# Optimization experiments

Hardware: AMD Instinct MI355X
Metric: run time of the kernel (lower is better)

Reference implementation:

```python
import jax, jax.numpy as jnp
import numpy as np

B, S, E, NH = 2, 1024, 2048, 16
DH = E // NH
EPS = 1e-6

def setup_inputs() -> dict:
    key = jax.random.key(0)
    ks = jax.random.split(key, 6)
    q = jax.random.normal(ks[0], (B, S, E), dtype=jnp.float32)
    k = jax.random.normal(ks[1], (B, S, E), dtype=jnp.float32)
    v = jax.random.normal(ks[2], (B, S, E), dtype=jnp.float32)
    Wi = jax.random.normal(ks[3], (3 * E, NH), dtype=jnp.float32) * 0.02
    bi = jax.random.normal(ks[4], (NH,), dtype=jnp.float32) * 0.1
    Wf = jax.random.normal(ks[5], (3 * E, NH), dtype=jnp.float32) * 0.02
    bf = jnp.linspace(3.0, 6.0, NH, dtype=jnp.float32)  # bias_linspace_initializer(3,6)
    ln_scale = jnp.ones((E,), dtype=jnp.float32)
    return {"q": q, "k": k, "v": v, "Wi": Wi, "bi": bi, "Wf": Wf, "bf": bf, "ln_scale": ln_scale}

def _mlstm_forward(q, k, v, Wi, bi, Wf, bf, ln_scale):
    b, s, e = q.shape
    nh = Wi.shape[1]
    dh = e // nh
    x = jnp.concatenate([q, k, v], axis=-1)                     # (B,S,3E)
    ig = (x @ Wi + bi).transpose(0, 2, 1)[..., None]            # (B,NH,S,1)
    fg = (x @ Wf + bf).transpose(0, 2, 1)[..., None]            # (B,NH,S,1)
    split = lambda t: t.reshape(b, s, nh, dh).transpose(0, 2, 1, 3)
    qh, kh, vh = split(q), split(k), split(v)                   # (B,NH,S,DH)
    # parallel_stabilized_simple backend
    log_f = jax.nn.log_sigmoid(fg)                              # (B,NH,S,1)
    log_f_cum = jnp.concatenate(
        [jnp.zeros((b, nh, 1, 1), q.dtype), jnp.cumsum(log_f, axis=2)], axis=2
    )                                                           # (B,NH,S+1,1)
    # D[i,j] = cumsum[i] - cumsum[j] on causal part
    fg_mat = log_f_cum - jnp.transpose(log_f_cum, (0, 1, 3, 2)) # (B,NH,S+1,S+1)
    ltr = jnp.tril(jnp.ones((s, s), dtype=bool))
    log_fg = jnp.where(ltr, fg_mat[:, :, 1:, 1:], -jnp.inf)     # (B,NH,S,S)
    log_D = log_fg + jnp.transpose(ig, (0, 1, 3, 2))            # + i_j per column
    max_log_D = jnp.max(log_D, axis=-1, keepdims=True)          # (B,NH,S,1)
    D = jnp.exp(log_D - max_log_D)
    qk = jnp.einsum('bhsd,bhtd->bhst', qh, kh) / jnp.sqrt(jnp.asarray(dh, q.dtype))
    C = qk * D                                                  # (B,NH,S,S)
    normalizer = jnp.maximum(jnp.abs(C.sum(-1, keepdims=True)), jnp.exp(-max_log_D))
    Cn = C / (normalizer + EPS)
    h = jnp.einsum('bhst,bhtd->bhsd', Cn, vh)                   # (B,NH,S,DH)
    # MultiHeadLayerNorm: normalize over DH per head, scale (no bias)
    mu = h.mean(-1, keepdims=True)
    var = ((h - mu) ** 2).mean(-1, keepdims=True)
    hn = (h - mu) * jax.lax.rsqrt(var + EPS)
    hn = hn * ln_scale.reshape(1, nh, 1, dh)
    return hn.transpose(0, 2, 1, 3).reshape(b, s, e)            # (B,S,E)

def reference(q, k, v, Wi, bi, Wf, bf, ln_scale):
    return _mlstm_forward(q, k, v, Wi, bi, Wf, bf, ln_scale)
```

## Files before the change

### kernel.cpp

```cpp
#include <hip/hip_runtime.h>
#include <hip/hip_bf16.h>

#define B_   2
#define S_   1024
#define E_   2048
#define NH_  16
#define DH_  128
#define EPS_ 1e-6f

using half8   = __attribute__((ext_vector_type(8))) _Float16;
using floatx4 = __attribute__((ext_vector_type(4))) float;

__device__ __forceinline__ half8 cvt8h(const float* __restrict__ p) {
    float4 a = *(const float4*)p;
    float4 b = *(const float4*)(p + 4);
    half8 r;
    r[0] = (_Float16)a.x; r[1] = (_Float16)a.y;
    r[2] = (_Float16)a.z; r[3] = (_Float16)a.w;
    r[4] = (_Float16)b.x; r[5] = (_Float16)b.y;
    r[6] = (_Float16)b.z; r[7] = (_Float16)b.w;
    return r;
}

__global__ __launch_bounds__(256, 4) void gates_kernel(
    const float* __restrict__ q, const float* __restrict__ k,
    const float* __restrict__ v, const float* __restrict__ Wi,
    const float* __restrict__ Wf, float* __restrict__ pre_i,
    float* __restrict__ pre_f, _Float16* __restrict__ qhg,
    _Float16* __restrict__ khg, _Float16* __restrict__ vtg)
{
    __shared__ __attribute__((aligned(16))) _Float16 xs[32 * 264];
    __shared__ __attribute__((aligned(16))) _Float16 wt[32 * 264];

    const int t    = threadIdx.x;
    const int w    = t >> 6, lane = t & 63, quad = lane >> 4, l15 = lane & 15;
    const int mw   = w & 1, nw = w >> 1;
    const int m0   = blockIdx.x * 32;
    const int by   = blockIdx.y;
    const int kbase = by * 768;
    const int bblk = m0 >> 10;
    const int s0   = m0 & 1023;

    floatx4 acc = {0.f, 0.f, 0.f, 0.f};

    for (int c = 0; c < 3; ++c) {
        __syncthreads();
        const int e0   = kbase + c * 256;
        const int tsel = e0 >> 11;
        const int el0  = e0 & 2047;
        const float* xb = (tsel == 0) ? q : (tsel == 1) ? k : v;
        _Float16* fout = (tsel == 0) ? qhg : khg;
        #pragma unroll
        for (int i = 0; i < 4; ++i) {
            int g = t + i * 256;
            int row = g >> 5, grp = g & 31;
            half8 s8 = cvt8h(xb + (size_t)(m0 + row) * E_ + el0 + grp * 8);
            *(half8*)(&xs[row * 264 + grp * 8]) = s8;
            if (tsel < 2) {
                int el = el0 + grp * 8;
                int h  = el >> 7, d = el & 127;
                *(half8*)(fout + ((size_t)(bblk * NH_ + h) * S_ + s0 + row) * DH_ + d) = s8;
            }
        }
        {
            const int kk = t;
            const float* wiRow = Wi + (size_t)(e0 + kk) * NH_;
            const float* wfRow = Wf + (size_t)(e0 + kk) * NH_;
            float wif[16], wff[16];
            #pragma unroll
            for (int i4 = 0; i4 < 4; ++i4) {
                float4 a = *(const float4*)(wiRow + i4 * 4);
                wif[i4*4+0]=a.x; wif[i4*4+1]=a.y; wif[i4*4+2]=a.z; wif[i4*4+3]=a.w;
                float4 b = *(const float4*)(wfRow + i4 * 4);
                wff[i4*4+0]=b.x; wff[i4*4+1]=b.y; wff[i4*4+2]=b.z; wff[i4*4+3]=b.w;
            }
            #pragma unroll
            for (int hh = 0; hh < 16; ++hh) wt[hh * 264 + kk]        = (_Float16)wif[hh];
            #pragma unroll
            for (int hh = 0; hh < 16; ++hh) wt[(16 + hh) * 264 + kk] = (_Float16)wff[hh];
        }
        __syncthreads();
        if (tsel == 2) {
            const int col = t;
            const int el  = el0 + col;
            const int h   = el >> 7, d = el & 127;
            _Float16 tmp[32];
            #pragma unroll
            for (int r = 0; r < 32; ++r) tmp[r] = xs[r * 264 + col];
            const size_t vo = ((size_t)(bblk * NH_ + h) * DH_ + d) * S_ + s0;
            #pragma unroll
            for (int i = 0; i < 4; ++i)
                *(half8*)(vtg + vo + i * 8) = *(half8*)(&tmp[i * 8]);
        }
        #pragma unroll
        for (int ks = 0; ks < 8; ++ks) {
            half8 af = *(const half8*)(&xs[(mw * 16 + l15) * 264 + ks * 32 + quad * 8]);
            half8 bw = *(const half8*)(&wt[(nw * 16 + l15) * 264 + ks * 32 + quad * 8]);
            acc = __builtin_amdgcn_mfma_f32_16x16x32_f16(af, bw, acc, 0, 0, 0);
        }
    }
    #pragma unroll
    for (int reg = 0; reg < 4; ++reg) {
        int m   = m0 + mw * 16 + quad * 4 + reg;
        int b   = m >> 10, s = m & 1023;
        int col = nw * 16 + l15;
        float vacc = acc[reg];
        if (col < 16)
            pre_i[((size_t)(by * 32 + b * NH_ + col)) * S_ + s] = vacc;
        else
            pre_f[((size_t)(by * 32 + b * NH_ + col - 16)) * S_ + s] = vacc;
    }
}

__global__ __launch_bounds__(1024, 1) void scan_kernel(
    const float* __restrict__ pre_i, const float* __restrict__ pre_f,
    float* __restrict__ Aj, float* __restrict__ Cq,
    float* __restrict__ NFo, const float* __restrict__ bi,
    const float* __restrict__ bfb)
{
    __shared__ float wsumF[16], wmaxA[16];
    const int bh   = blockIdx.x;
    const int h    = bh & 15;
    const int t    = threadIdx.x;
    const int lane = t & 63, wv = t >> 6;

    float igv = bi[h], x = bfb[h];
    #pragma unroll
    for (int y = 0; y < 8; ++y) {
        igv += pre_i[((size_t)(y * 32 + bh)) * S_ + t];
        x   += pre_f[((size_t)(y * 32 + bh)) * S_ + t];
    }
    float lfv = (x >= 0.f) ? -log1pf(__expf(-x)) : (x - log1pf(__expf(x)));

    float sc = lfv;
    #pragma unroll
    for (int off = 1; off < 64; off <<= 1) {
        float o = __shfl_up(sc, off);
        if (lane >= off) sc += o;
    }
    if (lane == 63) wsumF[wv] = sc;
    __syncthreads();
    float Foff = 0.f;
    for (int i = 0; i < wv; ++i) Foff += wsumF[i];
    float F = Foff + sc;
    float a = igv - F;

    float ms = a;
    #pragma unroll
    for (int off = 1; off < 64; off <<= 1) {
        float o = __shfl_up(ms, off);
        if (lane >= off) ms = fmaxf(ms, o);
    }
    if (lane == 63) wmaxA[wv] = ms;
    __syncthreads();
    float Moff = -3.0e38f;
    for (int i = 0; i < wv; ++i) Moff = fmaxf(Moff, wmaxA[i]);
    float M = fmaxf(Moff, ms);

    size_t o = (size_t)bh * S_ + t;
    const float L2E = 1.4426950408889634f;
    Aj[o]  = a * L2E;
    Cq[o]  = -M * L2E - 3.5f;
    NFo[o] = expf(fminf(-(F + M), 80.f));
}

__global__ __launch_bounds__(256, 2) void attn_kernel(
    const _Float16* __restrict__ qh, const _Float16* __restrict__ kh,
    const _Float16* __restrict__ vtg, const float* __restrict__ Aj,
    const float* __restrict__ Cq, const float* __restrict__ NFi,
    const float* __restrict__ lnsc, float* __restrict__ out)
{
    __shared__ __attribute__((aligned(16))) _Float16 Ks[64 * 136];
    __shared__ __attribute__((aligned(16))) _Float16 Vt[128 * 72];
    __shared__ __attribute__((aligned(16))) _Float16 Pb[64 * 72];
    __shared__ float aj[64];
    __shared__ float lpart[2][2][32];
    __shared__ float spart[2][2][32];
    __shared__ float qpart[2][2][32];

    const int t    = threadIdx.x;
    const int w    = t >> 6, lane = t & 63, quad = lane >> 4, l15 = lane & 15;
    const int mw   = w & 1, nw = w >> 1;
    const int L    = blockIdx.x;
    int qi, bh;
    if (L < 256) { qi = L >> 5;                bh = L & 31; }
    else         { qi = 15 - ((L - 256) >> 5); bh = (L - 256) & 31; }
    const int b    = bh >> 4, h = bh & 15;
    const int q0   = qi * 64;
    const int krow = t >> 2, kd0 = (t & 3) * 32;
    const int vd   = t >> 1, vj0 = (t & 1) * 32;

    float ci_r[2][4], nfv_r[2][4];
    #pragma unroll
    for (int s = 0; s < 2; ++s)
        #pragma unroll
        for (int reg = 0; reg < 4; ++reg) {
            int rl = q0 + mw * 32 + s * 16 + quad * 4 + reg;
            ci_r[s][reg]  = Cq[(size_t)bh * S_ + rl];
            nfv_r[s][reg] = NFi[(size_t)bh * S_ + rl];
        }
    half8 aq[2][4];
    #pragma unroll
    for (int s = 0; s < 2; ++s) {
        const _Float16* qrow = qh + ((size_t)bh * S_ + q0 + mw * 32 + s * 16 + l15) * DH_;
        #pragma unroll
        for (int ks = 0; ks < 4; ++ks)
            aq[s][ks] = *(const half8*)(qrow + ks * 32 + quad * 8);
    }

    half8 kreg[4], vreg[4];
    float ajreg = 0.f;
    {
        const _Float16* kp = kh + ((size_t)bh * S_ + krow) * DH_ + kd0;
        const _Float16* vp = vtg + ((size_t)bh * DH_ + vd) * S_ + vj0;
        #pragma unroll
        for (int i = 0; i < 4; ++i) { kreg[i] = *(const half8*)(kp + i * 8);
                                      vreg[i] = *(const half8*)(vp + i * 8); }
    }
    if (t < 64) ajreg = Aj[(size_t)bh * S_ + t];

    #pragma unroll
    for (int i = 0; i < 4; ++i) {
        *(half8*)(&Ks[krow * 136 + kd0 + i * 8]) = kreg[i];
        *(half8*)(&Vt[vd * 72 + vj0 + i * 8])    = vreg[i];
    }
    if (t < 64) aj[t] = ajreg;
    __syncthreads();

    floatx4 acc_h[2][4];
    #pragma unroll
    for (int s = 0; s < 2; ++s)
        #pragma unroll
        for (int i = 0; i < 4; ++i) acc_h[s][i] = (floatx4){0.f, 0.f, 0.f, 0.f};
    float lrun[2][4] = {{0.f, 0.f, 0.f, 0.f}, {0.f, 0.f, 0.f, 0.f}};

    for (int kt = 0; kt <= qi; ++kt) {
        if (kt < qi) {
            const int j0n = (kt + 1) * 64;
            const _Float16* kp = kh + ((size_t)bh * S_ + j0n + krow) * DH_ + kd0;
            const _Float16* vp = vtg + ((size_t)bh * DH_ + vd) * S_ + j0n + vj0;
            #pragma unroll
            for (int i = 0; i < 4; ++i) { kreg[i] = *(const half8*)(kp + i * 8);
                                          vreg[i] = *(const half8*)(vp + i * 8); }
            if (t < 64) ajreg = Aj[(size_t)bh * S_ + j0n + t];
        }

        const bool diag = (kt == qi);
        floatx4 sacc[2][2];
        #pragma unroll
        for (int s = 0; s < 2; ++s)
            #pragma unroll
            for (int n = 0; n < 2; ++n) sacc[s][n] = (floatx4){0.f, 0.f, 0.f, 0.f};
        if (!(diag && mw == 0 && nw == 1)) {
            __builtin_amdgcn_s_setprio(1);
            #pragma unroll
            for (int ks = 0; ks < 4; ++ks) {
                #pragma unroll
                for (int n = 0; n < 2; ++n) {
                    half8 bk = *(const half8*)(&Ks[(nw * 32 + n * 16 + l15) * 136 + ks * 32 + quad * 8]);
                    sacc[0][n] = __builtin_amdgcn_mfma_f32_16x16x32_f16(aq[0][ks], bk, sacc[0][n], 0, 0, 0);
                    sacc[1][n] = __builtin_amdgcn_mfma_f32_16x16x32_f16(aq[1][ks], bk, sacc[1][n], 0, 0, 0);
                }
            }
            __builtin_amdgcn_s_setprio(0);
        }
        #pragma unroll
        for (int n = 0; n < 2; ++n) {
            int jl = nw * 32 + n * 16 + l15;
            float a_j = aj[jl];
            #pragma unroll
            for (int s = 0; s < 2; ++s) {
                #pragma unroll
                for (int reg = 0; reg < 4; ++reg) {
                    int rloc = mw * 32 + s * 16 + quad * 4 + reg;
                    float p = 0.f;
                    if (!diag || (jl <= rloc))
                        p = sacc[s][n][reg] * exp2f(ci_r[s][reg] + a_j);
                    lrun[s][reg] += p;
                    Pb[rloc * 72 + jl] = (_Float16)p;
                }
            }
        }
        __syncthreads();

        if (kt < qi) {
            #pragma unroll
            for (int i = 0; i < 4; ++i)
                *(half8*)(&Ks[krow * 136 + kd0 + i * 8]) = kreg[i];
            if (t < 64) aj[t] = ajreg;
        }
        __builtin_amdgcn_s_setprio(1);
        #pragma unroll
        for (int ks2 = 0; ks2 < 2; ++ks2) {
            half8 ap0 = *(const half8*)(&Pb[(mw * 32 + l15) * 72 + ks2 * 32 + quad * 8]);
            half8 ap1 = *(const half8*)(&Pb[(mw * 32 + 16 + l15) * 72 + ks2 * 32 + quad * 8]);
            #pragma unroll
            for (int n = 0; n < 4; ++n) {
                half8 bv = *(const half8*)(&Vt[(nw * 64 + n * 16 + l15) * 72 + ks2 * 32 + quad * 8]);
                acc_h[0][n] = __builtin_amdgcn_mfma_f32_16x16x32_f16(ap0, bv, acc_h[0][n], 0, 0, 0);
                acc_h[1][n] = __builtin_amdgcn_mfma_f32_16x16x32_f16(ap1, bv, acc_h[1][n], 0, 0, 0);
            }
        }
        __builtin_amdgcn_s_setprio(0);
        __syncthreads();

        if (kt < qi) {
            #pragma unroll
            for (int i = 0; i < 4; ++i)
                *(half8*)(&Vt[vd * 72 + vj0 + i * 8]) = vreg[i];
        }
    }

    #pragma unroll
    for (int s = 0; s < 2; ++s)
        #pragma unroll
        for (int reg = 0; reg < 4; ++reg) {
            float l = lrun[s][reg];
            l += __shfl_xor(l, 1); l += __shfl_xor(l, 2);
            l += __shfl_xor(l, 4); l += __shfl_xor(l, 8);
            if (l15 == 0) lpart[nw][mw][s * 16 + quad * 4 + reg] = l;
        }
    __syncthreads();
    float inv_r[2][4];
    #pragma unroll
    for (int s = 0; s < 2; ++s)
        #pragma unroll
        for (int reg = 0; reg < 4; ++reg) {
            int rr = s * 16 + quad * 4 + reg;
            float ltot = lpart[0][mw][rr] + lpart[1][mw][rr];
            inv_r[s][reg] = 1.f / (fmaxf(fabsf(ltot), nfv_r[s][reg]) + EPS_);
        }
    #pragma unroll
    for (int s = 0; s < 2; ++s)
        #pragma unroll
        for (int reg = 0; reg < 4; ++reg) {
            float sum = 0.f, sq = 0.f;
            #pragma unroll
            for (int n = 0; n < 4; ++n) {
                float x = acc_h[s][n][reg] * inv_r[s][reg];
                sum += x; sq += x * x;
            }
            sum += __shfl_xor(sum, 1); sq += __shfl_xor(sq, 1);
            sum += __shfl_xor(sum, 2); sq += __shfl_xor(sq, 2);
            sum += __shfl_xor(sum, 4); sq += __shfl_xor(sq, 4);
            sum += __shfl_xor(sum, 8); sq += __shfl_xor(sq, 8);
            if (l15 == 0) {
                spart[nw][mw][s * 16 + quad * 4 + reg] = sum;
                qpart[nw][mw][s * 16 + quad * 4 + reg] = sq;
            }
        }
    __syncthreads();
    #pragma unroll
    for (int s = 0; s < 2; ++s)
        #pragma unroll
        for (int reg = 0; reg < 4; ++reg) {
            int rr   = s * 16 + quad * 4 + reg;
            float sum = spart[0][mw][rr] + spart[1][mw][rr];
            float sq  = qpart[0][mw][rr] + qpart[1][mw][rr];
            float mean = sum * (1.f / 128.f);
            float var  = fmaxf(sq * (1.f / 128.f) - mean * mean, 0.f);
            float rstd = rsqrtf(var + EPS_);
            int rl = q0 + mw * 32 + rr;
            size_t orow = ((size_t)b * S_ + rl) * E_ + h * DH_;
            #pragma unroll
            for (int n = 0; n < 4; ++n) {
                int d = nw * 64 + n * 16 + l15;
                out[orow + d] = (acc_h[s][n][reg] * inv_r[s][reg] - mean) * rstd * lnsc[h * DH_ + d];
            }
        }
}

extern "C" void kernel_launch(void* const* d_in, const int* in_sizes, int n_in,
                              void* d_out, int out_size, void* d_ws, size_t ws_size,
                              hipStream_t stream)
{
    const float* q    = (const float*)d_in[0];
    const float* k    = (const float*)d_in[1];
    const float* v    = (const float*)d_in[2];
    const float* Wi   = (const float*)d_in[3];
    const float* bi   = (const float*)d_in[4];
    const float* Wf   = (const float*)d_in[5];
    const float* bfb  = (const float*)d_in[6];
    const float* lnsc = (const float*)d_in[7];
    float* out        = (float*)d_out;

    const int NS  = B_ * NH_ * S_;
    float* pre_i = (float*)d_ws;
    float* pre_f = pre_i + 8 * NS;
    float* Aj    = pre_f + 8 * NS;
    float* Cq    = Aj + NS;
    float* NFa   = Cq + NS;
    _Float16* qh  = (_Float16*)(NFa + NS);
    _Float16* kh  = qh + (size_t)32 * S_ * DH_;
    _Float16* vtg = kh + (size_t)32 * S_ * DH_;

    gates_kernel<<<dim3(64, 8), 256, 0, stream>>>(q, k, v, Wi, Wf, pre_i, pre_f,
                                                  qh, kh, vtg);
    scan_kernel<<<dim3(32), 1024, 0, stream>>>(pre_i, pre_f, Aj, Cq, NFa, bi, bfb);
    attn_kernel<<<dim3(512), 256, 0, stream>>>(qh, kh, vtg, Aj, Cq, NFa, lnsc, out);
}
```

Before: 146.4 us.

## Split heavy causal query tiles across two blocks with partial-sum combine kernel

The attention kernel now handles query tiles 8-15 (the ones with the most key tiles) with two blocks, each covering half of the key range. Both blocks write their unnormalized accumulators and row sums to a workspace, and a new attn_fin kernel adds the two halves and applies normalization plus the layer norm. This evens out per-block work across 768 blocks to shorten the tail. The cost is an extra kernel launch and a workspace round trip for the partial results.

```diff
diff --git a/kernel.cpp b/kernel.cpp
--- a/kernel.cpp
+++ b/kernel.cpp
@@ -164,11 +164,12 @@
     NFo[o] = expf(fminf(-(F + M), 80.f));
 }
 
-__global__ __launch_bounds__(256, 2) void attn_kernel(
+__global__ __launch_bounds__(256, 2) void attn_part(
     const _Float16* __restrict__ qh, const _Float16* __restrict__ kh,
     const _Float16* __restrict__ vtg, const float* __restrict__ Aj,
     const float* __restrict__ Cq, const float* __restrict__ NFi,
-    const float* __restrict__ lnsc, float* __restrict__ out)
+    const float* __restrict__ lnsc, float* __restrict__ out,
+    float* __restrict__ pws)
 {
     __shared__ __attribute__((aligned(16))) _Float16 Ks[64 * 136];
     __shared__ __attribute__((aligned(16))) _Float16 Vt[128 * 72];
@@ -182,11 +183,20 @@
     const int w    = t >> 6, lane = t & 63, quad = lane >> 4, l15 = lane & 15;
     const int mw   = w & 1, nw = w >> 1;
     const int L    = blockIdx.x;
-    int qi, bh;
-    if (L < 256) { qi = L >> 5;                bh = L & 31; }
-    else         { qi = 15 - ((L - 256) >> 5); bh = (L - 256) & 31; }
+    int bh, qt, k0, k1;
+    bool light;
+    if (L < 256) {
+        bh = L & 31; qt = L >> 5; k0 = 0; k1 = qt + 1; light = true;
+    } else {
+        const int u = L & 255;
+        bh = u & 31; qt = 15 - (u >> 5);
+        const int nt = qt + 1, hA = (nt + 1) >> 1;
+        if (L < 512) { k0 = 0;  k1 = hA; }
+        else         { k0 = hA; k1 = nt; }
+        light = false;
+    }
     const int b    = bh >> 4, h = bh & 15;
-    const int q0   = qi * 64;
+    const int q0   = qt * 64;
     const int krow = t >> 2, kd0 = (t & 3) * 32;
     const int vd   = t >> 1, vj0 = (t & 1) * 32;
 
@@ -211,13 +221,14 @@
     half8 kreg[4], vreg[4];
     float ajreg = 0.f;
     {
-        const _Float16* kp = kh + ((size_t)bh * S_ + krow) * DH_ + kd0;
-        const _Float16* vp = vtg + ((size_t)bh * DH_ + vd) * S_ + vj0;
+        const int j00 = k0 * 64;
+        const _Float16* kp = kh + ((size_t)bh * S_ + j00 + krow) * DH_ + kd0;
+        const _Float16* vp = vtg + ((size_t)bh * DH_ + vd) * S_ + j00 + vj0;
         #pragma unroll
         for (int i = 0; i < 4; ++i) { kreg[i] = *(const half8*)(kp + i * 8);
                                       vreg[i] = *(const half8*)(vp + i * 8); }
-    }
-    if (t < 64) ajreg = Aj[(size_t)bh * S_ + t];
+        if (t < 64) ajreg = Aj[(size_t)bh * S_ + j00 + t];
+    }
 
     #pragma unroll
     for (int i = 0; i < 4; ++i) {
@@ -234,8 +245,8 @@
         for (int i = 0; i < 4; ++i) acc_h[s][i] = (floatx4){0.f, 0.f, 0.f, 0.f};
     float lrun[2][4] = {{0.f, 0.f, 0.f, 0.f}, {0.f, 0.f, 0.f, 0.f}};
 
-    for (int kt = 0; kt <= qi; ++kt) {
-        if (kt < qi) {
+    for (int kt = k0; kt < k1; ++kt) {
+        if (kt + 1 < k1) {
             const int j0n = (kt + 1) * 64;
             const _Float16* kp = kh + ((size_t)bh * S_ + j0n + krow) * DH_ + kd0;
             const _Float16* vp = vtg + ((size_t)bh * DH_ + vd) * S_ + j0n + vj0;
@@ -245,7 +256,7 @@
             if (t < 64) ajreg = Aj[(size_t)bh * S_ + j0n + t];
         }
 
-        const bool diag = (kt == qi);
+        const bool diag = (kt == qt);
         floatx4 sacc[2][2];
         #pragma unroll
         for (int s = 0; s < 2; ++s)
@@ -283,7 +294,7 @@
         }
         __syncthreads();
 
-        if (kt < qi) {
+        if (kt + 1 < k1) {
             #pragma unroll
             for (int i = 0; i < 4; ++i)
                 *(half8*)(&Ks[krow * 136 + kd0 + i * 8]) = kreg[i];
@@ -304,12 +315,132 @@
         __builtin_amdgcn_s_setprio(0);
         __syncthreads();
 
-        if (kt < qi) {
+        if (kt + 1 < k1) {
             #pragma unroll
             for (int i = 0; i < 4; ++i)
                 *(half8*)(&Vt[vd * 72 + vj0 + i * 8]) = vreg[i];
         }
     }
+
+    if (!light) {
+        const int slot = (bh * 8 + (qt - 8)) * 2 + (L >= 512 ? 1 : 0);
+        #pragma unroll
+        for (int s = 0; s < 2; ++s)
+            #pragma unroll
+            for (int n = 0; n < 4; ++n) {
+                int i = s * 4 + n;
+                *(floatx4*)(pws + (((size_t)slot * 10 + i) * 256 + t) * 4) = acc_h[s][n];
+            }
+        #pragma unroll
+        for (int s = 0; s < 2; ++s) {
+            floatx4 lv = {lrun[s][0], lrun[s][1], lrun[s][2], lrun[s][3]};
+            *(floatx4*)(pws + (((size_t)slot * 10 + 8 + s) * 256 + t) * 4) = lv;
+        }
+        return;
+    }
+
+    #pragma unroll
+    for (int s = 0; s < 2; ++s)
+        #pragma unroll
+        for (int reg = 0; reg < 4; ++reg) {
+            float l = lrun[s][reg];
+            l += __shfl_xor(l, 1); l += __shfl_xor(l, 2);
+            l += __shfl_xor(l, 4); l += __shfl_xor(l, 8);
+            if (l15 == 0) lpart[nw][mw][s * 16 + quad * 4 + reg] = l;
+        }
+    __syncthreads();
+    float inv_r[2][4];
+    #pragma unroll
+    for (int s = 0; s < 2; ++s)
+        #pragma unroll
+        for (int reg = 0; reg < 4; ++reg) {
+            int rr = s * 16 + quad * 4 + reg;
+            float ltot = lpart[0][mw][rr] + lpart[1][mw][rr];
+            inv_r[s][reg] = 1.f / (fmaxf(fabsf(ltot), nfv_r[s][reg]) + EPS_);
+        }
+    #pragma unroll
+    for (int s = 0; s < 2; ++s)
+        #pragma unroll
+        for (int reg = 0; reg < 4; ++reg) {
+            float sum = 0.f, sq = 0.f;
+            #pragma unroll
+            for (int n = 0; n < 4; ++n) {
+                float x = acc_h[s][n][reg] * inv_r[s][reg];
+                sum += x; sq += x * x;
+            }
+            sum += __shfl_xor(sum, 1); sq += __shfl_xor(sq, 1);
+            sum += __shfl_xor(sum, 2); sq += __shfl_xor(sq, 2);
+            sum += __shfl_xor(sum, 4); sq += __shfl_xor(sq, 4);
+            sum += __shfl_xor(sum, 8); sq += __shfl_xor(sq, 8);
+            if (l15 == 0) {
+                spart[nw][mw][s * 16 + quad * 4 + reg] = sum;
+                qpart[nw][mw][s * 16 + quad * 4 + reg] = sq;
+            }
+        }
+    __syncthreads();
+    #pragma unroll
+    for (int s = 0; s < 2; ++s)
+        #pragma unroll
+        for (int reg = 0; reg < 4; ++reg) {
+            int rr   = s * 16 + quad * 4 + reg;
+            float sum = spart[0][mw][rr] + spart[1][mw][rr];
+            float sq  = qpart[0][mw][rr] + qpart[1][mw][rr];
+            float mean = sum * (1.f / 128.f);
+            float var  = fmaxf(sq * (1.f / 128.f) - mean * mean, 0.f);
+            float rstd = rsqrtf(var + EPS_);
+            int rl = q0 + mw * 32 + rr;
+            size_t orow = ((size_t)b * S_ + rl) * E_ + h * DH_;
+            #pragma unroll
+            for (int n = 0; n < 4; ++n) {
+                int d = nw * 64 + n * 16 + l15;
+                out[orow + d] = (acc_h[s][n][reg] * inv_r[s][reg] - mean) * rstd * lnsc[h * DH_ + d];
+            }
+        }
+}
+
+__global__ __launch_bounds__(256, 4) void attn_fin(
+    const float* __restrict__ pws, const float* __restrict__ NFi,
+    const float* __restrict__ lnsc, float* __restrict__ out)
+{
+    __shared__ float lpart[2][2][32];
+    __shared__ float spart[2][2][32];
+    __shared__ float qpart[2][2][32];
+
+    const int t    = threadIdx.x;
+    const int w    = t >> 6, lane = t & 63, quad = lane >> 4, l15 = lane & 15;
+    const int mw   = w & 1, nw = w >> 1;
+    const int p    = blockIdx.x;
+    const int bh   = p >> 3, qt = (p & 7) + 8;
+    const int b    = bh >> 4, h = bh & 15;
+    const int q0   = qt * 64;
+    const int slotA = p * 2, slotB = p * 2 + 1;
+
+    floatx4 acc_h[2][4];
+    float lrun[2][4];
+    #pragma unroll
+    for (int s = 0; s < 2; ++s)
+        #pragma unroll
+        for (int n = 0; n < 4; ++n) {
+            int i = s * 4 + n;
+            floatx4 va = *(const floatx4*)(pws + (((size_t)slotA * 10 + i) * 256 + t) * 4);
+            floatx4 vb = *(const floatx4*)(pws + (((size_t)slotB * 10 + i) * 256 + t) * 4);
+            acc_h[s][n] = va + vb;
+        }
+    #pragma unroll
+    for (int s = 0; s < 2; ++s) {
+        floatx4 la = *(const floatx4*)(pws + (((size_t)slotA * 10 + 8 + s) * 256 + t) * 4);
+        floatx4 lb = *(const floatx4*)(pws + (((size_t)slotB * 10 + 8 + s) * 256 + t) * 4);
+        lrun[s][0] = la[0] + lb[0]; lrun[s][1] = la[1] + lb[1];
+        lrun[s][2] = la[2] + lb[2]; lrun[s][3] = la[3] + lb[3];
+    }
+    float nfv_r[2][4];
+    #pragma unroll
+    for (int s = 0; s < 2; ++s)
+        #pragma unroll
+        for (int reg = 0; reg < 4; ++reg) {
+            int rl = q0 + mw * 32 + s * 16 + quad * 4 + reg;
+            nfv_r[s][reg] = NFi[(size_t)bh * S_ + rl];
+        }
 
     #pragma unroll
     for (int s = 0; s < 2; ++s)
@@ -393,9 +524,12 @@
     _Float16* qh  = (_Float16*)(NFa + NS);
     _Float16* kh  = qh + (size_t)32 * S_ * DH_;
     _Float16* vtg = kh + (size_t)32 * S_ * DH_;
+    float* pws    = (float*)(vtg + (size_t)32 * DH_ * S_);
 
     gates_kernel<<<dim3(64, 8), 256, 0, stream>>>(q, k, v, Wi, Wf, pre_i, pre_f,
                                                   qh, kh, vtg);
     scan_kernel<<<dim3(32), 1024, 0, stream>>>(pre_i, pre_f, Aj, Cq, NFa, bi, bfb);
-    attn_kernel<<<dim3(512), 256, 0, stream>>>(qh, kh, vtg, Aj, Cq, NFa, lnsc, out);
+    attn_part<<<dim3(768), 256, 0, stream>>>(qh, kh, vtg, Aj, Cq, NFa, lnsc,
+                                             out, pws);
+    attn_fin<<<dim3(256), 256, 0, stream>>>(pws, NFa, lnsc, out);
 }
```

Measured after the change: 150.5 us. 2.8% more time.

## Double-buffer K and P tiles in LDS and load V fragments directly into registers

Applied to the files above, without the earlier changes.

The attention loop now keeps V operands in registers, loaded straight from global memory in MFMA fragment layout and ping-ponged between two register sets, so the V staging through shared memory goes away. K, P and the aj scalars are double-buffered in LDS, which removes the second __syncthreads per key tile. The goal is less LDS traffic and fewer barriers per iteration. The cost is more VGPRs (two V fragment sets of 8 half8 each) and more LDS for the doubled K and P buffers, which may lower occupancy under the 256,2 launch bounds.

```diff
diff --git a/kernel.cpp b/kernel.cpp
--- a/kernel.cpp
+++ b/kernel.cpp
@@ -170,10 +170,9 @@
     const float* __restrict__ Cq, const float* __restrict__ NFi,
     const float* __restrict__ lnsc, float* __restrict__ out)
 {
-    __shared__ __attribute__((aligned(16))) _Float16 Ks[64 * 136];
-    __shared__ __attribute__((aligned(16))) _Float16 Vt[128 * 72];
-    __shared__ __attribute__((aligned(16))) _Float16 Pb[64 * 72];
-    __shared__ float aj[64];
+    __shared__ __attribute__((aligned(16))) _Float16 Ks[2][64 * 136];
+    __shared__ __attribute__((aligned(16))) _Float16 Pb[2][64 * 72];
+    __shared__ float aj[2][64];
     __shared__ float lpart[2][2][32];
     __shared__ float spart[2][2][32];
     __shared__ float qpart[2][2][32];
@@ -188,7 +187,8 @@
     const int b    = bh >> 4, h = bh & 15;
     const int q0   = qi * 64;
     const int krow = t >> 2, kd0 = (t & 3) * 32;
-    const int vd   = t >> 1, vj0 = (t & 1) * 32;
+
+    const _Float16* vfb = vtg + ((size_t)bh * DH_ + nw * 64 + l15) * S_ + quad * 8;
 
     float ci_r[2][4], nfv_r[2][4];
     #pragma unroll
@@ -208,23 +208,24 @@
             aq[s][ks] = *(const half8*)(qrow + ks * 32 + quad * 8);
     }
 
-    half8 kreg[4], vreg[4];
+    half8 kreg[4];
+    half8 vA[2][4], vB[2][4];
     float ajreg = 0.f;
     {
         const _Float16* kp = kh + ((size_t)bh * S_ + krow) * DH_ + kd0;
-        const _Float16* vp = vtg + ((size_t)bh * DH_ + vd) * S_ + vj0;
-        #pragma unroll
-        for (int i = 0; i < 4; ++i) { kreg[i] = *(const half8*)(kp + i * 8);
-                                      vreg[i] = *(const half8*)(vp + i * 8); }
+        #pragma unroll
+        for (int i = 0; i < 4; ++i) kreg[i] = *(const half8*)(kp + i * 8);
+        #pragma unroll
+        for (int n = 0; n < 4; ++n)
+            #pragma unroll
+            for (int ks2 = 0; ks2 < 2; ++ks2)
+                vA[ks2][n] = *(const half8*)(vfb + n * 16 * S_ + ks2 * 32);
     }
     if (t < 64) ajreg = Aj[(size_t)bh * S_ + t];
-
-    #pragma unroll
-    for (int i = 0; i < 4; ++i) {
-        *(half8*)(&Ks[krow * 136 + kd0 + i * 8]) = kreg[i];
-        *(half8*)(&Vt[vd * 72 + vj0 + i * 8])    = vreg[i];
-    }
-    if (t < 64) aj[t] = ajreg;
+    #pragma unroll
+    for (int i = 0; i < 4; ++i)
+        *(half8*)(&Ks[0][krow * 136 + kd0 + i * 8]) = kreg[i];
+    if (t < 64) aj[0][t] = ajreg;
     __syncthreads();
 
     floatx4 acc_h[2][4];
@@ -234,18 +235,24 @@
         for (int i = 0; i < 4; ++i) acc_h[s][i] = (floatx4){0.f, 0.f, 0.f, 0.f};
     float lrun[2][4] = {{0.f, 0.f, 0.f, 0.f}, {0.f, 0.f, 0.f, 0.f}};
 
-    for (int kt = 0; kt <= qi; ++kt) {
-        if (kt < qi) {
+    auto tile_body = [&](int kt, half8 (&vcur)[2][4], half8 (&vnxt)[2][4]) {
+        const bool haveNext = (kt < qi);
+        if (haveNext) {
             const int j0n = (kt + 1) * 64;
             const _Float16* kp = kh + ((size_t)bh * S_ + j0n + krow) * DH_ + kd0;
-            const _Float16* vp = vtg + ((size_t)bh * DH_ + vd) * S_ + j0n + vj0;
-            #pragma unroll
-            for (int i = 0; i < 4; ++i) { kreg[i] = *(const half8*)(kp + i * 8);
-                                          vreg[i] = *(const half8*)(vp + i * 8); }
+            #pragma unroll
+            for (int i = 0; i < 4; ++i) kreg[i] = *(const half8*)(kp + i * 8);
+            const _Float16* vp = vfb + j0n;
+            #pragma unroll
+            for (int n = 0; n < 4; ++n)
+                #pragma unroll
+                for (int ks2 = 0; ks2 < 2; ++ks2)
+                    vnxt[ks2][n] = *(const half8*)(vp + n * 16 * S_ + ks2 * 32);
             if (t < 64) ajreg = Aj[(size_t)bh * S_ + j0n + t];
         }
 
         const bool diag = (kt == qi);
+        const _Float16* ksb = &Ks[kt & 1][0];
         floatx4 sacc[2][2];
         #pragma unroll
         for (int s = 0; s < 2; ++s)
@@ -257,17 +264,19 @@
             for (int ks = 0; ks < 4; ++ks) {
                 #pragma unroll
                 for (int n = 0; n < 2; ++n) {
-                    half8 bk = *(const half8*)(&Ks[(nw * 32 + n * 16 + l15) * 136 + ks * 32 + quad * 8]);
+                    half8 bk = *(const half8*)(&ksb[(nw * 32 + n * 16 + l15) * 136 + ks * 32 + quad * 8]);
                     sacc[0][n] = __builtin_amdgcn_mfma_f32_16x16x32_f16(aq[0][ks], bk, sacc[0][n], 0, 0, 0);
                     sacc[1][n] = __builtin_amdgcn_mfma_f32_16x16x32_f16(aq[1][ks], bk, sacc[1][n], 0, 0, 0);
                 }
             }
             __builtin_amdgcn_s_setprio(0);
         }
+        _Float16* pb = &Pb[kt & 1][0];
+        const float* ajc = aj[kt & 1];
         #pragma unroll
         for (int n = 0; n < 2; ++n) {
             int jl = nw * 32 + n * 16 + l15;
-            float a_j = aj[jl];
+            float a_j = ajc[jl];
             #pragma unroll
             for (int s = 0; s < 2; ++s) {
                 #pragma unroll
@@ -277,38 +286,35 @@
                     if (!diag || (jl <= rloc))
                         p = sacc[s][n][reg] * exp2f(ci_r[s][reg] + a_j);
                     lrun[s][reg] += p;
-                    Pb[rloc * 72 + jl] = (_Float16)p;
+                    pb[rloc * 72 + jl] = (_Float16)p;
                 }
             }
         }
+        if (haveNext) {
+            #pragma unroll
+            for (int i = 0; i < 4; ++i)
+                *(half8*)(&Ks[(kt + 1) & 1][krow * 136 + kd0 + i * 8]) = kreg[i];
+            if (t < 64) aj[(kt + 1) & 1][t] = ajreg;
+        }
         __syncthreads();
 
-        if (kt < qi) {
-            #pragma unroll
-            for (int i = 0; i < 4; ++i)
-                *(half8*)(&Ks[krow * 136 + kd0 + i * 8]) = kreg[i];
-            if (t < 64) aj[t] = ajreg;
-        }
         __builtin_amdgcn_s_setprio(1);
         #pragma unroll
         for (int ks2 = 0; ks2 < 2; ++ks2) {
-            half8 ap0 = *(const half8*)(&Pb[(mw * 32 + l15) * 72 + ks2 * 32 + quad * 8]);
-            half8 ap1 = *(const half8*)(&Pb[(mw * 32 + 16 + l15) * 72 + ks2 * 32 + quad * 8]);
+            half8 ap0 = *(const half8*)(&pb[(mw * 32 + l15) * 72 + ks2 * 32 + quad * 8]);
+            half8 ap1 = *(const half8*)(&pb[(mw * 32 + 16 + l15) * 72 + ks2 * 32 + quad * 8]);
             #pragma unroll
             for (int n = 0; n < 4; ++n) {
-                half8 bv = *(const half8*)(&Vt[(nw * 64 + n * 16 + l15) * 72 + ks2 * 32 + quad * 8]);
-                acc_h[0][n] = __builtin_amdgcn_mfma_f32_16x16x32_f16(ap0, bv, acc_h[0][n], 0, 0, 0);
-                acc_h[1][n] = __builtin_amdgcn_mfma_f32_16x16x32_f16(ap1, bv, acc_h[1][n], 0, 0, 0);
+                acc_h[0][n] = __builtin_amdgcn_mfma_f32_16x16x32_f16(ap0, vcur[ks2][n], acc_h[0][n], 0, 0, 0);
+                acc_h[1][n] = __builtin_amdgcn_mfma_f32_16x16x32_f16(ap1, vcur[ks2][n], acc_h[1][n], 0, 0, 0);
             }
         }
         __builtin_amdgcn_s_setprio(0);
-        __syncthreads();
-
-        if (kt < qi) {
-            #pragma unroll
-            for (int i = 0; i < 4; ++i)
-                *(half8*)(&Vt[vd * 72 + vj0 + i * 8]) = vreg[i];
-        }
+    };
+
+    for (int kt = 0; kt <= qi; kt += 2) {
+        tile_body(kt, vA, vB);
+        if (kt + 1 <= qi) tile_body(kt + 1, vB, vA);
     }
 
     #pragma unroll
```

Result: slower. 150.7 us (+2.9%).
